# Kernel tuning notes

Hardware: AMD Instinct MI355X
Metric: run time of the kernel (lower is better)

Reference implementation:

```python
import jax, jax.numpy as jnp
import numpy as np

NEG_BIG = -9e15

def setup_inputs() -> dict:
    key = jax.random.key(0)
    k1, k2, k3, k4 = jax.random.split(key, 4)
    N, Fin, Fout = 8192, 256, 128
    x = jax.random.normal(k1, (N, Fin), dtype=jnp.float32)
    adj = jax.random.randint(k2, (N, N), 0, 2, dtype=jnp.int32)
    # xavier-uniform-like init
    limW = float(np.sqrt(6.0 / (Fin + Fout)))
    W = jax.random.uniform(k3, (Fin, Fout), minval=-limW, maxval=limW, dtype=jnp.float32)
    lima = float(np.sqrt(6.0 / (2 * Fout + 1)))
    a = jax.random.uniform(k4, (2 * Fout, 1), minval=-lima, maxval=lima, dtype=jnp.float32)
    return {"x": x, "adj": adj, "W": W, "a": a}

def reference(x, adj, W, a, alpha=0.2):
    # h: (N, Fout)
    h = x @ W
    Fout = W.shape[1]
    # Split a into source/target halves: e[i,j] = leakyrelu(h_i·a1 + h_j·a2)
    a1, a2 = a[:Fout, 0], a[Fout:, 0]
    s = h @ a1  # (N,) row (source) scores
    t = h @ a2  # (N,) col (target) scores
    e = jax.nn.leaky_relu(s[:, None] + t[None, :], negative_slope=alpha)  # (N, N)
    e = jnp.where(adj > 0, e, NEG_BIG)
    attention = jax.nn.softmax(e, axis=1)
    # dropout omitted (eval mode / training=False)
    return attention @ h
```

## Files before the change

kernel.cpp:

```cpp
#include <hip/hip_runtime.h>
#include <hip/hip_bf16.h>

typedef __attribute__((ext_vector_type(8))) short short8;
typedef __attribute__((ext_vector_type(4))) short short4v;
typedef __attribute__((ext_vector_type(4))) float f32x4;

#define NR 8192
#define LOG2E 1.4426950408889634f

__device__ __forceinline__ short f2bf(float f) {
  return __builtin_bit_cast(short, __float2bfloat16(f));
}

__global__ __launch_bounds__(256) void k_pack(const int* __restrict__ adj,
                                              unsigned* __restrict__ mask) {
  size_t gid = (size_t)blockIdx.x * 256 + threadIdx.x;
  const int4* p = (const int4*)&adj[gid * 32];
  unsigned m = 0;
#pragma unroll
  for (int c = 0; c < 8; ++c) {
    int4 v = p[c];
    m |= (unsigned)(v.x > 0) << (c * 4 + 0);
    m |= (unsigned)(v.y > 0) << (c * 4 + 1);
    m |= (unsigned)(v.z > 0) << (c * 4 + 2);
    m |= (unsigned)(v.w > 0) << (c * 4 + 3);
  }
  mask[gid] = m;
}

__global__ __launch_bounds__(256) void k_gemm_h(const float* __restrict__ x,
                                                const float* __restrict__ W,
                                                const float* __restrict__ a,
                                                short* __restrict__ HT,
                                                float* __restrict__ sv,
                                                float* __restrict__ tv) {
  __shared__ short WT[128][136];
  const int tid = threadIdx.x;
  const int w = tid >> 6;
  const int L = tid & 63;
  const int lm = L & 15;
  const int q = L >> 4;
  const int i0 = blockIdx.x * 64;

  f32x4 acc[8];
#pragma unroll
  for (int nn = 0; nn < 8; ++nn) acc[nn] = (f32x4){0.f, 0.f, 0.f, 0.f};

  for (int kc = 0; kc < 256; kc += 128) {
    if (kc) __syncthreads();
#pragma unroll
    for (int p = 0; p < 16; ++p) {
      int idx = p * 256 + tid;
      int k = idx >> 5;
      int f4 = (idx & 31) * 4;
      float4 v = *(const float4*)&W[(kc + k) * 128 + f4];
      WT[f4 + 0][k] = f2bf(v.x);
      WT[f4 + 1][k] = f2bf(v.y);
      WT[f4 + 2][k] = f2bf(v.z);
      WT[f4 + 3][k] = f2bf(v.w);
    }
    __syncthreads();
#pragma unroll
    for (int ks = 0; ks < 4; ++ks) {
      int row = i0 + 16 * w + lm;
      const float* xp = &x[(size_t)row * 256 + kc + ks * 32 + q * 8];
      float4 xa = *(const float4*)xp;
      float4 xb = *(const float4*)(xp + 4);
      short8 af;
      af[0] = f2bf(xa.x); af[1] = f2bf(xa.y); af[2] = f2bf(xa.z); af[3] = f2bf(xa.w);
      af[4] = f2bf(xb.x); af[5] = f2bf(xb.y); af[6] = f2bf(xb.z); af[7] = f2bf(xb.w);
#pragma unroll
      for (int nn = 0; nn < 8; ++nn) {
        short8 bf = *(const short8*)&WT[nn * 16 + lm][ks * 32 + q * 8];
        acc[nn] = __builtin_amdgcn_mfma_f32_16x16x32_bf16(af, bf, acc[nn], 0, 0, 0);
      }
    }
  }

  const int ib = i0 + 16 * w + 4 * q;
  float a1v[8], a2v[8];
#pragma unroll
  for (int nn = 0; nn < 8; ++nn) {
    a1v[nn] = a[nn * 16 + lm];
    a2v[nn] = a[128 + nn * 16 + lm];
  }
  float sr[4] = {0.f, 0.f, 0.f, 0.f};
  float tr[4] = {0.f, 0.f, 0.f, 0.f};
#pragma unroll
  for (int nn = 0; nn < 8; ++nn) {
    int f = nn * 16 + lm;
    short4v o;
    o[0] = f2bf(acc[nn][0]);
    o[1] = f2bf(acc[nn][1]);
    o[2] = f2bf(acc[nn][2]);
    o[3] = f2bf(acc[nn][3]);
    *(short4v*)&HT[(size_t)f * NR + ib] = o;
#pragma unroll
    for (int r = 0; r < 4; ++r) {
      sr[r] += acc[nn][r] * a1v[nn];
      tr[r] += acc[nn][r] * a2v[nn];
    }
  }
#pragma unroll
  for (int d = 1; d < 16; d <<= 1) {
#pragma unroll
    for (int r = 0; r < 4; ++r) {
      sr[r] += __shfl_xor(sr[r], d);
      tr[r] += __shfl_xor(tr[r], d);
    }
  }
  if (lm == 0) {
#pragma unroll
    for (int r = 0; r < 4; ++r) {
      sv[ib + r] = sr[r] * LOG2E;
      tv[ib + r] = tr[r] * LOG2E;
    }
  }
}

__global__ __launch_bounds__(256, 2) void k_flash(const unsigned* __restrict__ mask,
                                                  const short* __restrict__ HT,
                                                  const float* __restrict__ sv,
                                                  const float* __restrict__ tv,
                                                  float* __restrict__ part,
                                                  float* __restrict__ lpart,
                                                  int S) {
  __shared__ float eps[4][32 * 128];
  const int tid = threadIdx.x;
  const int w = tid >> 6;
  const int L = tid & 63;
  const int lm = L & 15;
  const int q = L >> 4;
  const int nit = 64;
  const int sp = blockIdx.x / nit;
  const int it = blockIdx.x % nit;
  const int i0 = it * 128;

  const int row0 = i0 + 32 * w + lm;
  const int row1 = row0 + 16;
  const float s0 = sv[row0];
  const float s1 = sv[row1];

  f32x4 acc[2][8];
#pragma unroll
  for (int mm = 0; mm < 2; ++mm)
#pragma unroll
    for (int nn = 0; nn < 8; ++nn) acc[mm][nn] = (f32x4){0.f, 0.f, 0.f, 0.f};
  float l0 = 0.f, l1 = 0.f;

  const int JR = NR / S;
  const int j0 = sp * JR;
  const int ngroups = JR >> 7;
  const int w0base = row0 * 256 + (j0 >> 5);
  const int w1base = row1 * 256 + (j0 >> 5);

  for (int jg = 0; jg < ngroups; ++jg) {
    uint4 mw0 = *(const uint4*)&mask[w0base + jg * 4];
    uint4 mw1 = *(const uint4*)&mask[w1base + jg * 4];
    unsigned mwa0[4] = {mw0.x, mw0.y, mw0.z, mw0.w};
    unsigned mwa1[4] = {mw1.x, mw1.y, mw1.z, mw1.w};
#pragma unroll
    for (int jk = 0; jk < 4; ++jk) {
      const int jb = j0 + (jg * 4 + jk) * 32 + q * 8;
      float4 t0 = *(const float4*)&tv[jb];
      float4 t1 = *(const float4*)&tv[jb + 4];
      short8 bf[8];
#pragma unroll
      for (int nn = 0; nn < 8; ++nn)
        bf[nn] = *(const short8*)&HT[(size_t)(nn * 16 + lm) * NR + jb];

      const unsigned b0 = (mwa0[jk] >> (q * 8)) & 0xffu;
      const unsigned b1 = (mwa1[jk] >> (q * 8)) & 0xffu;
      float tvl[8] = {t0.x, t0.y, t0.z, t0.w, t1.x, t1.y, t1.z, t1.w};
      short8 p0, p1;
#pragma unroll
      for (int e = 0; e < 8; ++e) {
        float v0 = s0 + tvl[e];
        float e0 = fmaxf(v0, 0.2f * v0);
        float pp0 = (b0 & (1u << e)) ? __builtin_amdgcn_exp2f(e0) : 0.f;
        l0 += pp0;
        p0[e] = f2bf(pp0);
        float v1 = s1 + tvl[e];
        float e1 = fmaxf(v1, 0.2f * v1);
        float pp1 = (b1 & (1u << e)) ? __builtin_amdgcn_exp2f(e1) : 0.f;
        l1 += pp1;
        p1[e] = f2bf(pp1);
      }
#pragma unroll
      for (int nn = 0; nn < 8; ++nn) {
        acc[0][nn] = __builtin_amdgcn_mfma_f32_16x16x32_bf16(p0, bf[nn], acc[0][nn], 0, 0, 0);
        acc[1][nn] = __builtin_amdgcn_mfma_f32_16x16x32_bf16(p1, bf[nn], acc[1][nn], 0, 0, 0);
      }
    }
  }

  float* my = eps[w];
#pragma unroll
  for (int mm = 0; mm < 2; ++mm)
#pragma unroll
    for (int nn = 0; nn < 8; ++nn)
#pragma unroll
      for (int r = 0; r < 4; ++r)
        my[(16 * mm + 4 * q + r) * 128 + nn * 16 + lm] = acc[mm][nn][r];
  float* ps = part + ((size_t)sp * NR + i0 + 32 * w) * 128;
#pragma unroll
  for (int c = 0; c < 16; ++c) {
    float4 v = *(float4*)&my[(c * 64 + L) * 4];
    *(float4*)&ps[(size_t)(c * 64 + L) * 4] = v;
  }

  l0 += __shfl_xor(l0, 16);
  l0 += __shfl_xor(l0, 32);
  l1 += __shfl_xor(l1, 16);
  l1 += __shfl_xor(l1, 32);
  if (q == 0) {
    lpart[sp * NR + row0] = l0;
    lpart[sp * NR + row1] = l1;
  }
}

__global__ __launch_bounds__(256) void k_reduce(const float* __restrict__ part,
                                                const float* __restrict__ lpart,
                                                float* __restrict__ out, int S) {
  int idx4 = blockIdx.x * 256 + threadIdx.x;
  int idx = idx4 * 4;
  int i = idx >> 7;
  float4 sum = {0.f, 0.f, 0.f, 0.f};
  for (int sp = 0; sp < S; ++sp) {
    float4 v = *(const float4*)&part[(size_t)sp * (NR * 128) + idx];
    sum.x += v.x; sum.y += v.y; sum.z += v.z; sum.w += v.w;
  }
  float l = 0.f;
  for (int sp = 0; sp < S; ++sp) l += lpart[sp * NR + i];
  float inv = (l > 0.f) ? 1.f / l : 0.f;
  float4 o = {sum.x * inv, sum.y * inv, sum.z * inv, sum.w * inv};
  *(float4*)&out[idx] = o;
}

extern "C" void kernel_launch(void* const* d_in, const int* in_sizes, int n_in,
                              void* d_out, int out_size, void* d_ws, size_t ws_size,
                              hipStream_t stream) {
  const float* x = (const float*)d_in[0];
  const int* adj = (const int*)d_in[1];
  const float* W = (const float*)d_in[2];
  const float* a = (const float*)d_in[3];
  float* out = (float*)d_out;

  char* ws = (char*)d_ws;
  short* HT = (short*)(ws + 0);
  float* sv = (float*)(ws + 2097152);
  float* tv = (float*)(ws + 2129920);
  float* lpart = (float*)(ws + 2162688);
  unsigned* mask = (unsigned*)(ws + 2686976);
  float* part = (float*)(ws + 11075584);

  int S = 8;
  while (S > 1 && (size_t)11075584 + (size_t)S * 4194304 > ws_size) S >>= 1;

  hipLaunchKernelGGL(k_pack, dim3((NR * NR / 32) / 256), dim3(256), 0, stream, adj, mask);
  hipLaunchKernelGGL(k_gemm_h, dim3(128), dim3(256), 0, stream, x, W, a, HT, sv, tv);
  hipLaunchKernelGGL(k_flash, dim3(64 * S), dim3(256), 0, stream, mask, HT, sv, tv,
                     part, lpart, S);
  hipLaunchKernelGGL(k_reduce, dim3((NR * 128) / 1024), dim3(256), 0, stream, part,
                     lpart, out, S);
}
```

Baseline: 469.1 us.

## Tile HT into contiguous 32-column blocks and prefetch in single-wave flash blocks

The transposed h matrix is now stored in tiles of 32 nodes x 128 features, so each flash iteration reads one contiguous 8 KB block instead of 128 strided rows. The flash kernel now runs 64-thread blocks, each owning 32 rows, so there are four times as many blocks. Each block software-prefetches the next tile's h fragment, t values and mask words one iteration ahead. The workspace split count S is fixed at 8 with no fallback for a smaller workspace, and holding the prefetch buffers in registers raises register pressure.

```diff
diff --git a/kernel.cpp b/kernel.cpp
--- a/kernel.cpp
+++ b/kernel.cpp
@@ -31,7 +31,7 @@
 __global__ __launch_bounds__(256) void k_gemm_h(const float* __restrict__ x,
                                                 const float* __restrict__ W,
                                                 const float* __restrict__ a,
-                                                short* __restrict__ HT,
+                                                short* __restrict__ HT2,
                                                 float* __restrict__ sv,
                                                 float* __restrict__ tv) {
   __shared__ short WT[128][136];
@@ -78,6 +78,7 @@
   }
 
   const int ib = i0 + 16 * w + 4 * q;
+  const int tbase = (ib >> 5) * 4096 + (ib & 31);
   float a1v[8], a2v[8];
 #pragma unroll
   for (int nn = 0; nn < 8; ++nn) {
@@ -94,7 +95,7 @@
     o[1] = f2bf(acc[nn][1]);
     o[2] = f2bf(acc[nn][2]);
     o[3] = f2bf(acc[nn][3]);
-    *(short4v*)&HT[(size_t)f * NR + ib] = o;
+    *(short4v*)&HT2[tbase + f * 32] = o;
 #pragma unroll
     for (int r = 0; r < 4; ++r) {
       sr[r] += acc[nn][r] * a1v[nn];
@@ -118,25 +119,21 @@
   }
 }
 
-__global__ __launch_bounds__(256, 2) void k_flash(const unsigned* __restrict__ mask,
-                                                  const short* __restrict__ HT,
-                                                  const float* __restrict__ sv,
-                                                  const float* __restrict__ tv,
-                                                  float* __restrict__ part,
-                                                  float* __restrict__ lpart,
-                                                  int S) {
-  __shared__ float eps[4][32 * 128];
-  const int tid = threadIdx.x;
-  const int w = tid >> 6;
-  const int L = tid & 63;
+__global__ __launch_bounds__(64, 2) void k_flash(const unsigned* __restrict__ mask,
+                                                 const short* __restrict__ HT2,
+                                                 const float* __restrict__ sv,
+                                                 const float* __restrict__ tv,
+                                                 float* __restrict__ part,
+                                                 float* __restrict__ lpart) {
+  __shared__ float eps[32 * 128];
+  const int L = threadIdx.x;
   const int lm = L & 15;
   const int q = L >> 4;
-  const int nit = 64;
-  const int sp = blockIdx.x / nit;
-  const int it = blockIdx.x % nit;
-  const int i0 = it * 128;
-
-  const int row0 = i0 + 32 * w + lm;
+  const int sp = blockIdx.x >> 8;
+  const int it = blockIdx.x & 255;
+  const int i0 = it * 32;
+
+  const int row0 = i0 + lm;
   const int row1 = row0 + 16;
   const float s0 = sv[row0];
   const float s1 = sv[row1];
@@ -148,65 +145,75 @@
     for (int nn = 0; nn < 8; ++nn) acc[mm][nn] = (f32x4){0.f, 0.f, 0.f, 0.f};
   float l0 = 0.f, l1 = 0.f;
 
-  const int JR = NR / S;
-  const int j0 = sp * JR;
-  const int ngroups = JR >> 7;
-  const int w0base = row0 * 256 + (j0 >> 5);
-  const int w1base = row1 * 256 + (j0 >> 5);
-
-  for (int jg = 0; jg < ngroups; ++jg) {
-    uint4 mw0 = *(const uint4*)&mask[w0base + jg * 4];
-    uint4 mw1 = *(const uint4*)&mask[w1base + jg * 4];
-    unsigned mwa0[4] = {mw0.x, mw0.y, mw0.z, mw0.w};
-    unsigned mwa1[4] = {mw1.x, mw1.y, mw1.z, mw1.w};
-#pragma unroll
-    for (int jk = 0; jk < 4; ++jk) {
-      const int jb = j0 + (jg * 4 + jk) * 32 + q * 8;
-      float4 t0 = *(const float4*)&tv[jb];
-      float4 t1 = *(const float4*)&tv[jb + 4];
-      short8 bf[8];
-#pragma unroll
-      for (int nn = 0; nn < 8; ++nn)
-        bf[nn] = *(const short8*)&HT[(size_t)(nn * 16 + lm) * NR + jb];
-
-      const unsigned b0 = (mwa0[jk] >> (q * 8)) & 0xffu;
-      const unsigned b1 = (mwa1[jk] >> (q * 8)) & 0xffu;
-      float tvl[8] = {t0.x, t0.y, t0.z, t0.w, t1.x, t1.y, t1.z, t1.w};
-      short8 p0, p1;
-#pragma unroll
-      for (int e = 0; e < 8; ++e) {
-        float v0 = s0 + tvl[e];
-        float e0 = fmaxf(v0, 0.2f * v0);
-        float pp0 = (b0 & (1u << e)) ? __builtin_amdgcn_exp2f(e0) : 0.f;
-        l0 += pp0;
-        p0[e] = f2bf(pp0);
-        float v1 = s1 + tvl[e];
-        float e1 = fmaxf(v1, 0.2f * v1);
-        float pp1 = (b1 & (1u << e)) ? __builtin_amdgcn_exp2f(e1) : 0.f;
-        l1 += pp1;
-        p1[e] = f2bf(pp1);
+  const int tile0 = sp * 32;
+  const short* tp = &HT2[tile0 * 4096 + (lm * 32 + q * 8)];
+  short8 sbf[8];
+#pragma unroll
+  for (int nn = 0; nn < 8; ++nn) sbf[nn] = *(const short8*)&tp[nn * 512];
+  float4 stv0 = *(const float4*)&tv[tile0 * 32 + q * 8];
+  float4 stv1 = *(const float4*)&tv[tile0 * 32 + q * 8 + 4];
+  uint4 mg0 = *(const uint4*)&mask[row0 * 256 + tile0];
+  uint4 mg1 = *(const uint4*)&mask[row1 * 256 + tile0];
+
+  unsigned mwa0[4], mwa1[4];
+#pragma unroll 4
+  for (int t = 0; t < 32; ++t) {
+    short8 bf[8];
+#pragma unroll
+    for (int nn = 0; nn < 8; ++nn) bf[nn] = sbf[nn];
+    float4 tv0 = stv0, tv1 = stv1;
+    if ((t & 3) == 0) {
+      mwa0[0] = mg0.x; mwa0[1] = mg0.y; mwa0[2] = mg0.z; mwa0[3] = mg0.w;
+      mwa1[0] = mg1.x; mwa1[1] = mg1.y; mwa1[2] = mg1.z; mwa1[3] = mg1.w;
+      if (t + 4 < 32) {
+        mg0 = *(const uint4*)&mask[row0 * 256 + tile0 + t + 4];
+        mg1 = *(const uint4*)&mask[row1 * 256 + tile0 + t + 4];
       }
-#pragma unroll
-      for (int nn = 0; nn < 8; ++nn) {
-        acc[0][nn] = __builtin_amdgcn_mfma_f32_16x16x32_bf16(p0, bf[nn], acc[0][nn], 0, 0, 0);
-        acc[1][nn] = __builtin_amdgcn_mfma_f32_16x16x32_bf16(p1, bf[nn], acc[1][nn], 0, 0, 0);
-      }
-    }
-  }
-
-  float* my = eps[w];
+    }
+    if (t + 1 < 32) {
+      const short* np = &HT2[(tile0 + t + 1) * 4096 + (lm * 32 + q * 8)];
+#pragma unroll
+      for (int nn = 0; nn < 8; ++nn) sbf[nn] = *(const short8*)&np[nn * 512];
+      stv0 = *(const float4*)&tv[(tile0 + t + 1) * 32 + q * 8];
+      stv1 = *(const float4*)&tv[(tile0 + t + 1) * 32 + q * 8 + 4];
+    }
+
+    const unsigned b0 = (mwa0[t & 3] >> (q * 8)) & 0xffu;
+    const unsigned b1 = (mwa1[t & 3] >> (q * 8)) & 0xffu;
+    float tvl[8] = {tv0.x, tv0.y, tv0.z, tv0.w, tv1.x, tv1.y, tv1.z, tv1.w};
+    short8 p0, p1;
+#pragma unroll
+    for (int e = 0; e < 8; ++e) {
+      float v0 = s0 + tvl[e];
+      float e0 = fmaxf(v0, 0.2f * v0);
+      float pp0 = (b0 & (1u << e)) ? __builtin_amdgcn_exp2f(e0) : 0.f;
+      l0 += pp0;
+      p0[e] = f2bf(pp0);
+      float v1 = s1 + tvl[e];
+      float e1 = fmaxf(v1, 0.2f * v1);
+      float pp1 = (b1 & (1u << e)) ? __builtin_amdgcn_exp2f(e1) : 0.f;
+      l1 += pp1;
+      p1[e] = f2bf(pp1);
+    }
+#pragma unroll
+    for (int nn = 0; nn < 8; ++nn) {
+      acc[0][nn] = __builtin_amdgcn_mfma_f32_16x16x32_bf16(p0, bf[nn], acc[0][nn], 0, 0, 0);
+      acc[1][nn] = __builtin_amdgcn_mfma_f32_16x16x32_bf16(p1, bf[nn], acc[1][nn], 0, 0, 0);
+    }
+  }
+
 #pragma unroll
   for (int mm = 0; mm < 2; ++mm)
 #pragma unroll
     for (int nn = 0; nn < 8; ++nn)
 #pragma unroll
       for (int r = 0; r < 4; ++r)
-        my[(16 * mm + 4 * q + r) * 128 + nn * 16 + lm] = acc[mm][nn][r];
-  float* ps = part + ((size_t)sp * NR + i0 + 32 * w) * 128;
+        eps[(16 * mm + 4 * q + r) * 128 + nn * 16 + lm] = acc[mm][nn][r];
+  float* pbase = part + ((size_t)sp * NR + i0) * 128;
 #pragma unroll
   for (int c = 0; c < 16; ++c) {
-    float4 v = *(float4*)&my[(c * 64 + L) * 4];
-    *(float4*)&ps[(size_t)(c * 64 + L) * 4] = v;
+    int idx = (c * 64 + L) * 4;
+    *(float4*)&pbase[idx] = *(const float4*)&eps[idx];
   }
 
   l0 += __shfl_xor(l0, 16);
@@ -247,20 +254,19 @@
   float* out = (float*)d_out;
 
   char* ws = (char*)d_ws;
-  short* HT = (short*)(ws + 0);
+  short* HT2 = (short*)(ws + 0);
   float* sv = (float*)(ws + 2097152);
   float* tv = (float*)(ws + 2129920);
   float* lpart = (float*)(ws + 2162688);
   unsigned* mask = (unsigned*)(ws + 2686976);
-  float* part = (float*)(ws + 11075584);
-
-  int S = 8;
-  while (S > 1 && (size_t)11075584 + (size_t)S * 4194304 > ws_size) S >>= 1;
+  float* part = (float*)(ws + 11599872);
+
+  const int S = 8;
 
   hipLaunchKernelGGL(k_pack, dim3((NR * NR / 32) / 256), dim3(256), 0, stream, adj, mask);
-  hipLaunchKernelGGL(k_gemm_h, dim3(128), dim3(256), 0, stream, x, W, a, HT, sv, tv);
-  hipLaunchKernelGGL(k_flash, dim3(64 * S), dim3(256), 0, stream, mask, HT, sv, tv,
-                     part, lpart, S);
+  hipLaunchKernelGGL(k_gemm_h, dim3(128), dim3(256), 0, stream, x, W, a, HT2, sv, tv);
+  hipLaunchKernelGGL(k_flash, dim3(256 * S), dim3(64), 0, stream, mask, HT2, sv, tv,
+                     part, lpart);
   hipLaunchKernelGGL(k_reduce, dim3((NR * 128) / 1024), dim3(256), 0, stream, part,
                      lpart, out, S);
 }
```

Result: faster. 440.9 us (-6.0%).
